# Performance work log

Hardware: AMD Instinct MI355X
Metric: run time of the kernel (lower is better)

Reference implementation:

```python
import jax, jax.numpy as jnp
import numpy as np

B, T, J, C = 8, 243, 17, 512
H = 8
HD = C // H  # 64
SCALE = HD ** -0.5


def setup_inputs() -> dict:
    key = jax.random.key(0)
    ks = jax.random.split(key, 6)
    x = jax.random.normal(ks[0], (B, T, J, C), dtype=jnp.float32)
    # external attention map, broadcast-compatible with [B,H,J,T,T]; make it row-normalized like a softmax
    am = jax.random.uniform(ks[1], (B, H, J, T, T), dtype=jnp.float32)
    att_map = am / jnp.sum(am, axis=-1, keepdims=True)
    weight = jax.random.uniform(ks[2], (1,), dtype=jnp.float32)
    w_qkv = jax.random.normal(ks[3], (3 * C, C), dtype=jnp.float32) * 0.02
    w_proj = jax.random.normal(ks[4], (C, C), dtype=jnp.float32) * 0.02
    b_proj = jax.random.normal(ks[5], (C,), dtype=jnp.float32) * 0.02
    return {"x": x, "att_map": att_map, "weight": weight,
            "w_qkv": w_qkv, "w_proj": w_proj, "b_proj": b_proj}


def reference(x, att_map, weight, w_qkv, w_proj, b_proj):
    b, t, j, c = x.shape
    h, hd = H, c // H
    # qkv projection (no bias): [B,T,J,3C] -> [3,B,H,T,J,hd]
    qkv = jnp.einsum('btjc,dc->btjd', x, w_qkv).reshape(b, t, j, 3, h, hd)
    qkv = jnp.transpose(qkv, (3, 0, 4, 1, 2, 5))
    q, k, v = qkv[0], qkv[1], qkv[2]
    # transpose T <-> J: attention runs over the temporal axis per joint
    qt = jnp.swapaxes(q, 2, 3)  # [B,H,J,T,hd]
    kt = jnp.swapaxes(k, 2, 3)
    vt = jnp.swapaxes(v, 2, 3)
    attn = jnp.einsum('bhjtc,bhjsc->bhjts', qt, kt) * SCALE  # [B,H,J,T,T]
    attn = jax.nn.softmax(attn, axis=-1)
    # blend with external attention map (dropout p=0.0 -> identity)
    attn = weight * attn + (1.0 - weight) * att_map
    out = jnp.einsum('bhjts,bhjsc->bhjtc', attn, vt)  # [B,H,J,T,hd]
    out = jnp.transpose(out, (0, 3, 2, 1, 4)).reshape(b, t, j, c)  # [B,T,J,C]
    out = out @ w_proj.T + b_proj
    return out
```

## Files before the change

### kernel.cpp

```cpp
#include <hip/hip_runtime.h>
#include <hip/hip_bf16.h>

#define B_ 8
#define T_ 243
#define J_ 17
#define C_ 512
#define H_ 8
#define HD_ 64
#define M_ (B_*T_*J_)
#define SCALE_ 0.125f
#define QKV_ELEMS (B_*H_*J_*T_*HD_)

typedef __attribute__((ext_vector_type(4))) float f32x4;
typedef __attribute__((ext_vector_type(8))) short bf16x8;

__device__ __forceinline__ ushort f2bf(float f) {
  union { float f; unsigned u; } v; v.f = f;
  unsigned r = v.u + 0x7FFFu + ((v.u >> 16) & 1u);
  return (ushort)(r >> 16);
}
__device__ __forceinline__ float bf2f(ushort u) {
  union { unsigned u; float f; } v; v.u = (unsigned)u << 16; return v.f;
}

__global__ __launch_bounds__(256) void cvt_kernel(const float* __restrict__ in,
                                                  ushort* __restrict__ out, int n8) {
  int i = blockIdx.x * 256 + threadIdx.x;
  if (i >= n8) return;
  const float4* p = (const float4*)in + (size_t)i * 2;
  float4 v0 = p[0], v1 = p[1];
  bf16x8 o;
  o[0] = (short)f2bf(v0.x); o[1] = (short)f2bf(v0.y);
  o[2] = (short)f2bf(v0.z); o[3] = (short)f2bf(v0.w);
  o[4] = (short)f2bf(v1.x); o[5] = (short)f2bf(v1.y);
  o[6] = (short)f2bf(v1.z); o[7] = (short)f2bf(v1.w);
  *(bf16x8*)(out + (size_t)i * 8) = o;
}

template<int EPI>
__global__ __launch_bounds__(256) void gemm_bt(
    const ushort* __restrict__ A, const ushort* __restrict__ Bm,
    ushort* __restrict__ qkvout, float* __restrict__ fout,
    const float* __restrict__ bias)
{
  __shared__ ushort As[128 * 64];
  __shared__ ushort Bs[128 * 64];
  const int tid = threadIdx.x;
  const int lane = tid & 63;
  const int lo = lane & 15, hi = lane >> 4;
  const int wave = tid >> 6;
  const int wr = wave >> 1, wc = wave & 1;
  const int mt = blockIdx.x, nt = blockIdx.y;

  f32x4 acc[4][4] = {};

  for (int ks = 0; ks < 8; ++ks) {
    const int k0 = ks * 64;
    bf16x8 ra[4], rb[4];
    #pragma unroll
    for (int i = 0; i < 4; ++i) {
      int c = tid + i * 256;
      int row = c >> 3, col8 = c & 7;
      int arow = mt * 128 + row; if (arow > M_ - 1) arow = M_ - 1;
      ra[i] = *(const bf16x8*)(A + (size_t)arow * 512 + k0 + col8 * 8);
      int brow = nt * 128 + row;
      rb[i] = *(const bf16x8*)(Bm + (size_t)brow * 512 + k0 + col8 * 8);
    }
    __syncthreads();
    #pragma unroll
    for (int i = 0; i < 4; ++i) {
      int c = tid + i * 256;
      int row = c >> 3, col8 = c & 7;
      int sc = col8 ^ (row & 7);
      *(bf16x8*)(As + row * 64 + sc * 8) = ra[i];
      *(bf16x8*)(Bs + row * 64 + sc * 8) = rb[i];
    }
    __syncthreads();
    #pragma unroll
    for (int kk = 0; kk < 2; ++kk) {
      bf16x8 af[4], bf[4];
      #pragma unroll
      for (int mf = 0; mf < 4; ++mf) {
        int row = wr * 64 + mf * 16 + lo;
        int sc = (kk * 4 + hi) ^ (row & 7);
        af[mf] = *(const bf16x8*)(As + row * 64 + sc * 8);
      }
      #pragma unroll
      for (int nf = 0; nf < 4; ++nf) {
        int row = wc * 64 + nf * 16 + lo;
        int sc = (kk * 4 + hi) ^ (row & 7);
        bf[nf] = *(const bf16x8*)(Bs + row * 64 + sc * 8);
      }
      #pragma unroll
      for (int mf = 0; mf < 4; ++mf)
        #pragma unroll
        for (int nf = 0; nf < 4; ++nf)
          acc[mf][nf] = __builtin_amdgcn_mfma_f32_16x16x32_bf16(af[mf], bf[nf], acc[mf][nf], 0, 0, 0);
    }
  }

  if (EPI == 0) {
    const int which = nt >> 2;
    const int h = (nt * 2 + wc) & 7;
    const float scale = (which == 0) ? SCALE_ : 1.0f;
    ushort* basep = qkvout + (size_t)which * QKV_ELEMS;
    #pragma unroll
    for (int mf = 0; mf < 4; ++mf) {
      #pragma unroll
      for (int i = 0; i < 4; ++i) {
        int r = mt * 128 + wr * 64 + mf * 16 + hi * 4 + i;
        if (r >= M_) continue;
        int b = r / (T_ * J_);
        int rem = r - b * (T_ * J_);
        int t = rem / J_;
        int j = rem - t * J_;
        size_t rowoff = (((size_t)(b * H_ + h) * J_ + j) * T_ + t) * HD_;
        #pragma unroll
        for (int nf = 0; nf < 4; ++nf) {
          int hd = nf * 16 + lo;
          basep[rowoff + hd] = f2bf(acc[mf][nf][i] * scale);
        }
      }
    }
  } else {
    #pragma unroll
    for (int mf = 0; mf < 4; ++mf) {
      #pragma unroll
      for (int i = 0; i < 4; ++i) {
        int r = mt * 128 + wr * 64 + mf * 16 + hi * 4 + i;
        if (r >= M_) continue;
        #pragma unroll
        for (int nf = 0; nf < 4; ++nf) {
          int n = nt * 128 + wc * 64 + nf * 16 + lo;
          fout[(size_t)r * C_ + n] = acc[mf][nf][i] + bias[n];
        }
      }
    }
  }
}

__global__ __launch_bounds__(256, 3) void flash_kernel(
    const ushort* __restrict__ q, const ushort* __restrict__ k,
    const ushort* __restrict__ v, const float* __restrict__ wptr,
    ushort* __restrict__ O2)
{
  __shared__ ushort Vt[64 * 256];
  __shared__ ushort Ps[64 * 128];
  __shared__ float red0[2][64];
  __shared__ float red1[2][64];

  const int tid = threadIdx.x;
  const int lane = tid & 63;
  const int lo = lane & 15, hi = lane >> 4;
  const int wave = tid >> 6;
  const int wr = wave >> 1, wc = wave & 1;
  const int bid = blockIdx.x;
  const int workid = (bid & 7) * 544 + (bid >> 3);
  const int bhj = workid >> 2, rt = workid & 3;
  const float w = wptr[0];
  const size_t kvbase = (size_t)bhj * (T_ * HD_);
  const int r0 = rt * 64;

  #pragma unroll
  for (int it = 0; it < 8; ++it) {
    int c = tid + it * 256;
    int s = c >> 3, hd0 = (c & 7) * 8;
    bf16x8 val = {};
    if (s < T_) val = *(const bf16x8*)(v + kvbase + (size_t)s * HD_ + hd0);
    #pragma unroll
    for (int e = 0; e < 8; ++e) {
      int row = hd0 + e;
      int chunk = (s >> 3) ^ (row & 7);
      Vt[row * 256 + chunk * 8 + (s & 7)] = (ushort)val[e];
    }
  }
  __syncthreads();

  bf16x8 aq[2][2];
  #pragma unroll
  for (int mf = 0; mf < 2; ++mf) {
    int t = r0 + wr * 32 + mf * 16 + lo; if (t > T_ - 1) t = T_ - 1;
    #pragma unroll
    for (int kk = 0; kk < 2; ++kk)
      aq[mf][kk] = *(const bf16x8*)(q + kvbase + (size_t)t * HD_ + kk * 32 + hi * 8);
  }

  f32x4 acc[2][8] = {};
  #pragma unroll
  for (int nf = 0; nf < 8; ++nf) {
    int s = wc * 128 + nf * 16 + lo; if (s > T_ - 1) s = T_ - 1;
    #pragma unroll
    for (int kk = 0; kk < 2; ++kk) {
      bf16x8 bk = *(const bf16x8*)(k + kvbase + (size_t)s * HD_ + kk * 32 + hi * 8);
      #pragma unroll
      for (int mf = 0; mf < 2; ++mf)
        acc[mf][nf] = __builtin_amdgcn_mfma_f32_16x16x32_bf16(aq[mf][kk], bk, acc[mf][nf], 0, 0, 0);
    }
  }

  float rmax[2][4];
  #pragma unroll
  for (int mf = 0; mf < 2; ++mf)
    #pragma unroll
    for (int i = 0; i < 4; ++i) {
      float m = -1e30f;
      #pragma unroll
      for (int nf = 0; nf < 8; ++nf) {
        int s = wc * 128 + nf * 16 + lo;
        if (s < T_) m = fmaxf(m, acc[mf][nf][i]);
      }
      rmax[mf][i] = m;
    }
  #pragma unroll
  for (int d = 1; d < 16; d <<= 1)
    #pragma unroll
    for (int mf = 0; mf < 2; ++mf)
      #pragma unroll
      for (int i = 0; i < 4; ++i)
        rmax[mf][i] = fmaxf(rmax[mf][i], __shfl_xor(rmax[mf][i], d, 64));
  if (lo == 0) {
    #pragma unroll
    for (int mf = 0; mf < 2; ++mf)
      #pragma unroll
      for (int i = 0; i < 4; ++i)
        red0[wc][wr * 32 + mf * 16 + hi * 4 + i] = rmax[mf][i];
  }
  __syncthreads();

  float rsum[2][4];
  #pragma unroll
  for (int mf = 0; mf < 2; ++mf)
    #pragma unroll
    for (int i = 0; i < 4; ++i) {
      float Mx = fmaxf(rmax[mf][i], red0[wc ^ 1][wr * 32 + mf * 16 + hi * 4 + i]);
      float ssum = 0.f;
      #pragma unroll
      for (int nf = 0; nf < 8; ++nf) {
        int s = wc * 128 + nf * 16 + lo;
        float e = 0.f;
        if (s < T_) e = __expf(acc[mf][nf][i] - Mx);
        acc[mf][nf][i] = e;
        ssum += e;
      }
      rsum[mf][i] = ssum;
    }
  #pragma unroll
  for (int d = 1; d < 16; d <<= 1)
    #pragma unroll
    for (int mf = 0; mf < 2; ++mf)
      #pragma unroll
      for (int i = 0; i < 4; ++i)
        rsum[mf][i] += __shfl_xor(rsum[mf][i], d, 64);
  if (lo == 0) {
    #pragma unroll
    for (int mf = 0; mf < 2; ++mf)
      #pragma unroll
      for (int i = 0; i < 4; ++i)
        red1[wc][wr * 32 + mf * 16 + hi * 4 + i] = rsum[mf][i];
  }
  __syncthreads();

  float pinv[2][4];
  #pragma unroll
  for (int mf = 0; mf < 2; ++mf)
    #pragma unroll
    for (int i = 0; i < 4; ++i) {
      float L = rsum[mf][i] + red1[wc ^ 1][wr * 32 + mf * 16 + hi * 4 + i];
      pinv[mf][i] = w / L;
    }

  f32x4 oacc[2][2] = {};
  #pragma unroll
  for (int h2 = 0; h2 < 2; ++h2) {
    __syncthreads();
    if (wc == h2) {
      #pragma unroll
      for (int mf = 0; mf < 2; ++mf)
        #pragma unroll
        for (int i = 0; i < 4; ++i) {
          int row_local = wr * 32 + mf * 16 + hi * 4 + i;
          float pw = pinv[mf][i];
          #pragma unroll
          for (int nf = 0; nf < 8; ++nf) {
            int s = h2 * 128 + nf * 16 + lo;
            float p = (s < T_) ? acc[mf][nf][i] * pw : 0.f;
            int s_local = nf * 16 + lo;
            int chunk = (s_local >> 3) ^ (row_local & 7);
            Ps[row_local * 128 + chunk * 8 + (s_local & 7)] = f2bf(p);
          }
        }
    }
    __syncthreads();
    #pragma unroll
    for (int kk = 0; kk < 4; ++kk) {
      bf16x8 ap[2], bv[2];
      #pragma unroll
      for (int mf = 0; mf < 2; ++mf) {
        int row = wr * 32 + mf * 16 + lo;
        int chunk = (kk * 4 + hi) ^ (row & 7);
        ap[mf] = *(const bf16x8*)(Ps + row * 128 + chunk * 8);
      }
      #pragma unroll
      for (int nf = 0; nf < 2; ++nf) {
        int row = wc * 32 + nf * 16 + lo;
        int chunk = ((h2 * 4 + kk) * 4 + hi) ^ (row & 7);
        bv[nf] = *(const bf16x8*)(Vt + row * 256 + chunk * 8);
      }
      #pragma unroll
      for (int mf = 0; mf < 2; ++mf)
        #pragma unroll
        for (int nf = 0; nf < 2; ++nf)
          oacc[mf][nf] = __builtin_amdgcn_mfma_f32_16x16x32_bf16(ap[mf], bv[nf], oacc[mf][nf], 0, 0, 0);
    }
  }

  #pragma unroll
  for (int mf = 0; mf < 2; ++mf)
    #pragma unroll
    for (int i = 0; i < 4; ++i) {
      int t = r0 + wr * 32 + mf * 16 + hi * 4 + i;
      if (t >= T_) continue;
      size_t rowoff = ((size_t)bhj * T_ + t) * HD_;
      #pragma unroll
      for (int nf = 0; nf < 2; ++nf) {
        int hd = wc * 32 + nf * 16 + lo;
        O2[rowoff + hd] = f2bf(oacc[mf][nf][i]);
      }
    }
}

__global__ __launch_bounds__(256, 4) void amv_kernel(
    const float* __restrict__ am, const ushort* __restrict__ v,
    const ushort* __restrict__ o2, const float* __restrict__ wptr,
    ushort* __restrict__ outO)
{
  __shared__ ushort Vt[64 * 256];

  const int tid = threadIdx.x;
  const int lane = tid & 63;
  const int lo = lane & 15, hi = lane >> 4;
  const int wave = tid >> 6;
  const int wr = wave >> 1, wc = wave & 1;
  const int bid = blockIdx.x;
  const int workid = (bid & 7) * 544 + (bid >> 3);
  const int bhj = workid >> 2, rt = workid & 3;
  const int bh = bhj / J_, j = bhj - bh * J_;
  const int b = bh >> 3, h = bh & 7;
  const float wb = 1.0f - wptr[0];
  const size_t kvbase = (size_t)bhj * (T_ * HD_);
  const int r0 = rt * 64;

  #pragma unroll
  for (int it = 0; it < 8; ++it) {
    int c = tid + it * 256;
    int s = c >> 3, hd0 = (c & 7) * 8;
    bf16x8 val = {};
    if (s < T_) val = *(const bf16x8*)(v + kvbase + (size_t)s * HD_ + hd0);
    #pragma unroll
    for (int e = 0; e < 8; ++e) {
      int row = hd0 + e;
      int chunk = (s >> 3) ^ (row & 7);
      Vt[row * 256 + chunk * 8 + (s & 7)] = (ushort)val[e];
    }
  }
  __syncthreads();

  const float* amrow[2];
  #pragma unroll
  for (int mf = 0; mf < 2; ++mf) {
    int t = r0 + wr * 32 + mf * 16 + lo; if (t > T_ - 1) t = T_ - 1;
    amrow[mf] = am + (size_t)bhj * (T_ * T_) + (size_t)t * T_;
  }

  f32x4 acc[2][2] = {};
  #pragma unroll
  for (int kk = 0; kk < 8; ++kk) {
    const int s8 = kk * 32 + hi * 8;
    bf16x8 aa[2];
    #pragma unroll
    for (int mf = 0; mf < 2; ++mf) {
      bf16x8 r;
      if (s8 + 7 <= T_ - 1) {
        #pragma unroll
        for (int e = 0; e < 8; ++e) r[e] = (short)f2bf(amrow[mf][s8 + e]);
      } else {
        #pragma unroll
        for (int e = 0; e < 8; ++e) {
          int s = s8 + e;
          r[e] = (s <= T_ - 1) ? (short)f2bf(amrow[mf][s]) : (short)0;
        }
      }
      aa[mf] = r;
    }
    bf16x8 bv[2];
    #pragma unroll
    for (int nf = 0; nf < 2; ++nf) {
      int row = wc * 32 + nf * 16 + lo;
      int chunk = (kk * 4 + hi) ^ (row & 7);
      bv[nf] = *(const bf16x8*)(Vt + row * 256 + chunk * 8);
    }
    #pragma unroll
    for (int mf = 0; mf < 2; ++mf)
      #pragma unroll
      for (int nf = 0; nf < 2; ++nf)
        acc[mf][nf] = __builtin_amdgcn_mfma_f32_16x16x32_bf16(aa[mf], bv[nf], acc[mf][nf], 0, 0, 0);
  }

  #pragma unroll
  for (int mf = 0; mf < 2; ++mf)
    #pragma unroll
    for (int i = 0; i < 4; ++i) {
      int t = r0 + wr * 32 + mf * 16 + hi * 4 + i;
      if (t >= T_) continue;
      size_t o2row = ((size_t)bhj * T_ + t) * HD_;
      size_t orow = ((size_t)(b * T_ + t) * J_ + j) * C_ + h * HD_;
      #pragma unroll
      for (int nf = 0; nf < 2; ++nf) {
        int hd = wc * 32 + nf * 16 + lo;
        outO[orow + hd] = f2bf(wb * acc[mf][nf][i] + bf2f(o2[o2row + hd]));
      }
    }
}

extern "C" void kernel_launch(void* const* d_in, const int* in_sizes, int n_in,
                              void* d_out, int out_size, void* d_ws, size_t ws_size,
                              hipStream_t stream) {
  const float* x      = (const float*)d_in[0];
  const float* am     = (const float*)d_in[1];
  const float* weight = (const float*)d_in[2];
  const float* w_qkv  = (const float*)d_in[3];
  const float* w_proj = (const float*)d_in[4];
  const float* b_proj = (const float*)d_in[5];
  float* outp = (float*)d_out;

  char* ws = (char*)d_ws;
  ushort* wqkv_bf  = (ushort*)(ws);
  ushort* wproj_bf = (ushort*)(ws + 1572864);
  ushort* xbf      = (ushort*)(ws + 2097152);
  ushort* qws      = (ushort*)(ws + 35938304);
  ushort* kws = qws + QKV_ELEMS;
  ushort* vws = kws + QKV_ELEMS;
  if (ws_size < 137461760ull) return;

  cvt_kernel<<<8262, 256, 0, stream>>>(x, xbf, 2115072);
  cvt_kernel<<<384, 256, 0, stream>>>(w_qkv, wqkv_bf, 98304);
  cvt_kernel<<<128, 256, 0, stream>>>(w_proj, wproj_bf, 32768);

  gemm_bt<0><<<dim3(259, 12), 256, 0, stream>>>(xbf, wqkv_bf, qws, nullptr, nullptr);

  flash_kernel<<<4352, 256, 0, stream>>>(qws, kws, vws, weight, xbf);

  amv_kernel<<<4352, 256, 0, stream>>>(am, vws, xbf, weight, qws);

  gemm_bt<1><<<dim3(259, 4), 256, 0, stream>>>(qws, wproj_bf, nullptr, outp, b_proj);
}
```

Measured before the change: 369.4 us.

## Fuse attention and external-map times V kernels, improve V LDS swizzle

Merges the flash attention kernel and the att_map·V kernel into one kernel, so the V tile is loaded into shared memory once and the intermediate bf16 O2 buffer is no longer written and reread. The blend (w·softmax·V + (1-w)·att_map·V) is combined in registers before the single output store. The V-transpose LDS swizzle also XORs in higher row bits to cut bank conflicts. The cost is higher per-block register pressure under the existing launch bounds of 3 blocks, which may cause spills or lower occupancy for the fused att_map streaming phase.

```diff
diff --git a/kernel.cpp b/kernel.cpp
--- a/kernel.cpp
+++ b/kernel.cpp
@@ -21,6 +21,9 @@
 }
 __device__ __forceinline__ float bf2f(ushort u) {
   union { unsigned u; float f; } v; v.u = (unsigned)u << 16; return v.f;
+}
+__device__ __forceinline__ int vchunk(int g, int row) {
+  return g ^ (row & 7) ^ ((row >> 3) & 7);
 }
 
 __global__ __launch_bounds__(256) void cvt_kernel(const float* __restrict__ in,
@@ -139,10 +142,10 @@
   }
 }
 
-__global__ __launch_bounds__(256, 3) void flash_kernel(
+__global__ __launch_bounds__(256, 3) void attn_kernel(
     const ushort* __restrict__ q, const ushort* __restrict__ k,
-    const ushort* __restrict__ v, const float* __restrict__ wptr,
-    ushort* __restrict__ O2)
+    const ushort* __restrict__ v, const float* __restrict__ am,
+    const float* __restrict__ wptr, ushort* __restrict__ outO)
 {
   __shared__ ushort Vt[64 * 256];
   __shared__ ushort Ps[64 * 128];
@@ -157,7 +160,10 @@
   const int bid = blockIdx.x;
   const int workid = (bid & 7) * 544 + (bid >> 3);
   const int bhj = workid >> 2, rt = workid & 3;
+  const int bh = bhj / J_, j = bhj - bh * J_;
+  const int b = bh >> 3, h = bh & 7;
   const float w = wptr[0];
+  const float wb = 1.0f - w;
   const size_t kvbase = (size_t)bhj * (T_ * HD_);
   const int r0 = rt * 64;
 
@@ -170,7 +176,7 @@
     #pragma unroll
     for (int e = 0; e < 8; ++e) {
       int row = hd0 + e;
-      int chunk = (s >> 3) ^ (row & 7);
+      int chunk = vchunk(s >> 3, row);
       Vt[row * 256 + chunk * 8 + (s & 7)] = (ushort)val[e];
     }
   }
@@ -303,7 +309,7 @@
       #pragma unroll
       for (int nf = 0; nf < 2; ++nf) {
         int row = wc * 32 + nf * 16 + lo;
-        int chunk = ((h2 * 4 + kk) * 4 + hi) ^ (row & 7);
+        int chunk = vchunk((h2 * 4 + kk) * 4 + hi, row);
         bv[nf] = *(const bf16x8*)(Vt + row * 256 + chunk * 8);
       }
       #pragma unroll
@@ -313,57 +319,6 @@
           oacc[mf][nf] = __builtin_amdgcn_mfma_f32_16x16x32_bf16(ap[mf], bv[nf], oacc[mf][nf], 0, 0, 0);
     }
   }
-
-  #pragma unroll
-  for (int mf = 0; mf < 2; ++mf)
-    #pragma unroll
-    for (int i = 0; i < 4; ++i) {
-      int t = r0 + wr * 32 + mf * 16 + hi * 4 + i;
-      if (t >= T_) continue;
-      size_t rowoff = ((size_t)bhj * T_ + t) * HD_;
-      #pragma unroll
-      for (int nf = 0; nf < 2; ++nf) {
-        int hd = wc * 32 + nf * 16 + lo;
-        O2[rowoff + hd] = f2bf(oacc[mf][nf][i]);
-      }
-    }
-}
-
-__global__ __launch_bounds__(256, 4) void amv_kernel(
-    const float* __restrict__ am, const ushort* __restrict__ v,
-    const ushort* __restrict__ o2, const float* __restrict__ wptr,
-    ushort* __restrict__ outO)
-{
-  __shared__ ushort Vt[64 * 256];
-
-  const int tid = threadIdx.x;
-  const int lane = tid & 63;
-  const int lo = lane & 15, hi = lane >> 4;
-  const int wave = tid >> 6;
-  const int wr = wave >> 1, wc = wave & 1;
-  const int bid = blockIdx.x;
-  const int workid = (bid & 7) * 544 + (bid >> 3);
-  const int bhj = workid >> 2, rt = workid & 3;
-  const int bh = bhj / J_, j = bhj - bh * J_;
-  const int b = bh >> 3, h = bh & 7;
-  const float wb = 1.0f - wptr[0];
-  const size_t kvbase = (size_t)bhj * (T_ * HD_);
-  const int r0 = rt * 64;
-
-  #pragma unroll
-  for (int it = 0; it < 8; ++it) {
-    int c = tid + it * 256;
-    int s = c >> 3, hd0 = (c & 7) * 8;
-    bf16x8 val = {};
-    if (s < T_) val = *(const bf16x8*)(v + kvbase + (size_t)s * HD_ + hd0);
-    #pragma unroll
-    for (int e = 0; e < 8; ++e) {
-      int row = hd0 + e;
-      int chunk = (s >> 3) ^ (row & 7);
-      Vt[row * 256 + chunk * 8 + (s & 7)] = (ushort)val[e];
-    }
-  }
-  __syncthreads();
 
   const float* amrow[2];
   #pragma unroll
@@ -371,8 +326,7 @@
     int t = r0 + wr * 32 + mf * 16 + lo; if (t > T_ - 1) t = T_ - 1;
     amrow[mf] = am + (size_t)bhj * (T_ * T_) + (size_t)t * T_;
   }
-
-  f32x4 acc[2][2] = {};
+  f32x4 amacc[2][2] = {};
   #pragma unroll
   for (int kk = 0; kk < 8; ++kk) {
     const int s8 = kk * 32 + hi * 8;
@@ -396,14 +350,14 @@
     #pragma unroll
     for (int nf = 0; nf < 2; ++nf) {
       int row = wc * 32 + nf * 16 + lo;
-      int chunk = (kk * 4 + hi) ^ (row & 7);
+      int chunk = vchunk(kk * 4 + hi, row);
       bv[nf] = *(const bf16x8*)(Vt + row * 256 + chunk * 8);
     }
     #pragma unroll
     for (int mf = 0; mf < 2; ++mf)
       #pragma unroll
       for (int nf = 0; nf < 2; ++nf)
-        acc[mf][nf] = __builtin_amdgcn_mfma_f32_16x16x32_bf16(aa[mf], bv[nf], acc[mf][nf], 0, 0, 0);
+        amacc[mf][nf] = __builtin_amdgcn_mfma_f32_16x16x32_bf16(aa[mf], bv[nf], amacc[mf][nf], 0, 0, 0);
   }
 
   #pragma unroll
@@ -412,12 +366,11 @@
     for (int i = 0; i < 4; ++i) {
       int t = r0 + wr * 32 + mf * 16 + hi * 4 + i;
       if (t >= T_) continue;
-      size_t o2row = ((size_t)bhj * T_ + t) * HD_;
       size_t orow = ((size_t)(b * T_ + t) * J_ + j) * C_ + h * HD_;
       #pragma unroll
       for (int nf = 0; nf < 2; ++nf) {
         int hd = wc * 32 + nf * 16 + lo;
-        outO[orow + hd] = f2bf(wb * acc[mf][nf][i] + bf2f(o2[o2row + hd]));
+        outO[orow + hd] = f2bf(oacc[mf][nf][i] + wb * amacc[mf][nf][i]);
       }
     }
 }
@@ -448,9 +401,7 @@
 
   gemm_bt<0><<<dim3(259, 12), 256, 0, stream>>>(xbf, wqkv_bf, qws, nullptr, nullptr);
 
-  flash_kernel<<<4352, 256, 0, stream>>>(qws, kws, vws, weight, xbf);
-
-  amv_kernel<<<4352, 256, 0, stream>>>(am, vws, xbf, weight, qws);
-
-  gemm_bt<1><<<dim3(259, 4), 256, 0, stream>>>(qws, wproj_bf, nullptr, outp, b_proj);
-}
+  attn_kernel<<<4352, 256, 0, stream>>>(qws, kws, vws, am, weight, xbf);
+
+  gemm_bt<1><<<dim3(259, 4), 256, 0, stream>>>(xbf, wproj_bf, nullptr, outp, b_proj);
+}
```

After: 336.9 us. 8.8% less time.
